# Performance work log

Hardware: AMD Instinct MI355X
Metric: run time of the kernel (lower is better)

The kernel has to match this reference:

```python
import jax, jax.numpy as jnp
import numpy as np

EMBED = 1024
HEADS = 16
HEAD_DIM = EMBED // HEADS
HIDDEN = int(EMBED * 4.0)
EPS = 1e-6


def setup_inputs() -> dict:
    key = jax.random.key(0)
    ks = jax.random.split(key, 8)
    s = lambda fan_in: 1.0 / np.sqrt(fan_in)
    x = jax.random.normal(ks[0], (2, 2048, EMBED), dtype=jnp.float32)
    return {
        "x": x,
        "ln1_g": jnp.ones((EMBED,), jnp.float32),
        "ln1_b": jnp.zeros((EMBED,), jnp.float32),
        "w_qkv": jax.random.normal(ks[1], (EMBED, 3 * EMBED), jnp.float32) * s(EMBED),
        "b_qkv": jnp.zeros((3 * EMBED,), jnp.float32),
        "w_proj": jax.random.normal(ks[2], (EMBED, EMBED), jnp.float32) * s(EMBED),
        "b_proj": jnp.zeros((EMBED,), jnp.float32),
        "ln2_g": jnp.ones((EMBED,), jnp.float32),
        "ln2_b": jnp.zeros((EMBED,), jnp.float32),
        "w_fc1": jax.random.normal(ks[3], (EMBED, HIDDEN), jnp.float32) * s(EMBED),
        "b_fc1": jnp.zeros((HIDDEN,), jnp.float32),
        "w_fc2": jax.random.normal(ks[4], (HIDDEN, EMBED), jnp.float32) * s(HIDDEN),
        "b_fc2": jnp.zeros((EMBED,), jnp.float32),
    }


def _layernorm(x, g, b):
    mu = jnp.mean(x, axis=-1, keepdims=True)
    var = jnp.mean(jnp.square(x - mu), axis=-1, keepdims=True)
    return (x - mu) * jax.lax.rsqrt(var + EPS) * g + b


def _attention(x, w_qkv, b_qkv, w_proj, b_proj):
    B, N, C = x.shape
    qkv = x @ w_qkv + b_qkv                      # [B,N,3C]
    qkv = qkv.reshape(B, N, 3, HEADS, HEAD_DIM)
    q, k, v = (qkv[:, :, 0], qkv[:, :, 1], qkv[:, :, 2])  # [B,N,H,Dh]
    scale = HEAD_DIM ** -0.5
    attn = jnp.einsum('bnhd,bmhd->bhnm', q, k) * scale     # [B,H,N,N]
    attn = jax.nn.softmax(attn, axis=-1)
    out = jnp.einsum('bhnm,bmhd->bnhd', attn, v).reshape(B, N, C)
    return out @ w_proj + b_proj


def reference(x, ln1_g, ln1_b, w_qkv, b_qkv, w_proj, b_proj,
              ln2_g, ln2_b, w_fc1, b_fc1, w_fc2, b_fc2):
    x = x + _attention(_layernorm(x, ln1_g, ln1_b), w_qkv, b_qkv, w_proj, b_proj)
    h = _layernorm(x, ln2_g, ln2_b)
    h = jax.nn.gelu(h @ w_fc1 + b_fc1, approximate=False)
    x = x + (h @ w_fc2 + b_fc2)
    return x
```

## Files before the change

### kernel.cpp

```cpp
#include <hip/hip_runtime.h>
#include <hip/hip_bf16.h>
#include <math.h>

typedef __bf16 bf16x8 __attribute__((ext_vector_type(8)));
typedef __bf16 bf16x4 __attribute__((ext_vector_type(4)));
typedef unsigned short u16x8 __attribute__((ext_vector_type(8)));
typedef float f32x4 __attribute__((ext_vector_type(4)));

#define EP_QKV 0
#define EP_GELU 1
#define EP_RES 2

static __device__ __forceinline__ unsigned short f2bf(float x) {
  unsigned int u = __float_as_uint(x);
  unsigned int r = (u + 0x7fffu + ((u >> 16) & 1u)) >> 16;
  return (unsigned short)r;
}

static __device__ __forceinline__ unsigned int pkbf(float lo, float hi) {
  return __builtin_amdgcn_perm(__float_as_uint(hi), __float_as_uint(lo), 0x07060302);
}

static __device__ __forceinline__ void async16(const void* g, void* l) {
  __builtin_amdgcn_global_load_lds((__attribute__((address_space(1))) void*)g,
                                   (__attribute__((address_space(3))) void*)l, 16, 0, 0);
}

__global__ __launch_bounds__(256) void wt_transpose(const float* __restrict__ in,
                                                    unsigned short* __restrict__ out,
                                                    int K, int N) {
  __shared__ float tile[32][33];
  const int n0 = blockIdx.x * 32;
  const int k0 = blockIdx.y * 32;
  const int tx = threadIdx.x;
  const int ty = threadIdx.y;
  #pragma unroll
  for (int i = ty; i < 32; i += 8)
    tile[i][tx] = in[(size_t)(k0 + i) * N + n0 + tx];
  __syncthreads();
  #pragma unroll
  for (int i = ty; i < 32; i += 8)
    out[(size_t)(n0 + i) * K + k0 + tx] = f2bf(tile[tx][i]);
}

__global__ __launch_bounds__(256) void ln_kernel(const float* __restrict__ x,
                                                 const float* __restrict__ g,
                                                 const float* __restrict__ b,
                                                 unsigned short* __restrict__ outp) {
  const int row = blockIdx.x;
  const int tid = threadIdx.x;
  const int wave = tid >> 6, lane = tid & 63;
  const float4 v = ((const float4*)(x + (size_t)row * 1024))[tid];
  float s = v.x + v.y + v.z + v.w;
  #pragma unroll
  for (int i = 1; i < 64; i <<= 1) s += __shfl_xor(s, i);
  __shared__ float red[4];
  if (lane == 0) red[wave] = s;
  __syncthreads();
  const float mean = (red[0] + red[1] + red[2] + red[3]) * (1.f / 1024.f);
  const float dx = v.x - mean, dy = v.y - mean, dz = v.z - mean, dw = v.w - mean;
  float ss = dx * dx + dy * dy + dz * dz + dw * dw;
  #pragma unroll
  for (int i = 1; i < 64; i <<= 1) ss += __shfl_xor(ss, i);
  __syncthreads();
  if (lane == 0) red[wave] = ss;
  __syncthreads();
  const float var = (red[0] + red[1] + red[2] + red[3]) * (1.f / 1024.f);
  const float inv = rsqrtf(var + 1e-6f);
  const float4 gv = ((const float4*)g)[tid];
  const float4 bv = ((const float4*)b)[tid];
  ushort4 o;
  o.x = f2bf(dx * inv * gv.x + bv.x);
  o.y = f2bf(dy * inv * gv.y + bv.y);
  o.z = f2bf(dz * inv * gv.z + bv.z);
  o.w = f2bf(dw * inv * gv.w + bv.w);
  ((ushort4*)(outp + (size_t)row * 1024))[tid] = o;
}

template <int TN, int BK>
__global__ __launch_bounds__(256) void gemm_kernel(
    const unsigned short* __restrict__ A,
    const unsigned short* __restrict__ BT,
    const float* __restrict__ bias,
    int M, int N, int K, int mode,
    void* __restrict__ outp, const float* __restrict__ res) {
  constexpr int AM = (TN == 128) ? 4 : 2;
  constexpr int ACH = BK / 16;
  constexpr int BCH = TN * BK / 2048;
  constexpr int CPR = BK / 8;
  constexpr int ABYTES = 256 * BK;
  constexpr int BBYTES = TN * BK * 2;
  __shared__ __align__(16) char smem[2 * (ABYTES + BBYTES)];

  const int tid = threadIdx.x;
  const int wave = tid >> 6, lane = tid & 63;
  const int quad = lane >> 4, l16 = lane & 15;
  const int wm = (TN == 128) ? (wave >> 1) : wave;
  const int wn = (TN == 128) ? (wave & 1) : 0;

  const int nbm = M >> 7, nbn = N / TN;
  const int lin = blockIdx.y * gridDim.x + blockIdx.x;
  const int g = lin & 7, idx = lin >> 3;
  const int gm = nbm >> 2, gn = nbn >> 1;
  const int bm = (g & 3) * gm + (idx % gm);
  const int bn = (g >> 2) * gn + (idx / gm);
  const int row_m = bm * 128, row_n = bn * TN;

  int ar[ACH], ac[ACH];
  #pragma unroll
  for (int i = 0; i < ACH; ++i) {
    const int c = wave * (64 * ACH) + i * 64 + lane;
    ar[i] = c / CPR;
    ac[i] = ((c % CPR) ^ (ar[i] & (CPR - 1))) * 8;
  }
  int br[BCH], bc[BCH];
  #pragma unroll
  for (int i = 0; i < BCH; ++i) {
    const int c = wave * (64 * BCH) + i * 64 + lane;
    br[i] = c / CPR;
    bc[i] = ((c % CPR) ^ (br[i] & (CPR - 1))) * 8;
  }

  const unsigned short* Ag = A + (size_t)row_m * K;
  const unsigned short* Bg = BT + (size_t)row_n * K;

  const f32x4 z = {0.f, 0.f, 0.f, 0.f};
  f32x4 acc[AM][4];
  #pragma unroll
  for (int i = 0; i < AM; ++i)
    #pragma unroll
    for (int j = 0; j < 4; ++j) acc[i][j] = z;

  auto issue = [&](int kt, int b) {
    unsigned short* As = (unsigned short*)(smem + b * ABYTES);
    unsigned short* Bs = (unsigned short*)(smem + 2 * ABYTES + b * BBYTES);
    #pragma unroll
    for (int i = 0; i < ACH; ++i)
      async16(Ag + (size_t)ar[i] * K + kt + ac[i], As + wave * (ACH * 512) + i * 512);
    #pragma unroll
    for (int i = 0; i < BCH; ++i)
      async16(Bg + (size_t)br[i] * K + kt + bc[i], Bs + wave * (BCH * 512) + i * 512);
  };

  issue(0, 0);
  for (int kt = 0; kt < K; kt += BK) {
    const int b = (kt / BK) & 1;
    __syncthreads();
    if (kt + BK < K) issue(kt + BK, b ^ 1);
    const unsigned short* As = (const unsigned short*)(smem + b * ABYTES);
    const unsigned short* Bs = (const unsigned short*)(smem + 2 * ABYTES + b * BBYTES);
    #pragma unroll
    for (int h = 0; h < BK / 32; ++h) {
      bf16x8 af[AM], bfv[4];
      #pragma unroll
      for (int t = 0; t < AM; ++t) {
        const int row = wm * (AM * 16) + t * 16 + l16;
        const int ch = (h * 4 + quad) ^ (row & (CPR - 1));
        af[t] = *(const bf16x8*)(As + row * BK + ch * 8);
      }
      #pragma unroll
      for (int t = 0; t < 4; ++t) {
        const int row = wn * 64 + t * 16 + l16;
        const int ch = (h * 4 + quad) ^ (row & (CPR - 1));
        bfv[t] = *(const bf16x8*)(Bs + row * BK + ch * 8);
      }
      #pragma unroll
      for (int tm = 0; tm < AM; ++tm)
        #pragma unroll
        for (int tn = 0; tn < 4; ++tn)
          acc[tm][tn] = __builtin_amdgcn_mfma_f32_16x16x32_bf16(af[tm], bfv[tn], acc[tm][tn], 0, 0, 0);
    }
  }

  #pragma unroll
  for (int tn = 0; tn < 4; ++tn) {
    const int col = row_n + wn * 64 + tn * 16 + l16;
    const float bv = bias[col];
    #pragma unroll
    for (int tm = 0; tm < AM; ++tm) {
      const int rbase = row_m + wm * (AM * 16) + tm * 16 + quad * 4;
      float v[4];
      #pragma unroll
      for (int r = 0; r < 4; ++r) v[r] = acc[tm][tn][r] + bv;
      if (mode == EP_QKV) {
        unsigned short* outw = (unsigned short*)outp;
        const int which = col >> 10;
        const int h = (col >> 6) & 15, d = col & 63;
        const int bb = rbase >> 11, n = rbase & 2047;
        const size_t bh = (size_t)(bb * 16 + h);
        if (which == 0) {
          #pragma unroll
          for (int r = 0; r < 4; ++r)
            outw[(bh * 2048 + n + r) * 64 + d] = f2bf(v[r] * 0.18033688011112043f);
        } else if (which == 1) {
          #pragma unroll
          for (int r = 0; r < 4; ++r)
            outw[4194304ull + (bh * 2048 + n + r) * 64 + d] = f2bf(v[r]);
        } else {
          uint2 o;
          o.x = pkbf(v[0], v[1]);
          o.y = pkbf(v[2], v[3]);
          *(uint2*)(outw + 8388608ull + (bh * 64 + d) * 2048 + n) = o;
        }
      } else if (mode == EP_GELU) {
        #pragma unroll
        for (int r = 0; r < 4; ++r) {
          const float u = v[r];
          const float c = 1.5957691216f * fmaf(0.044715f * u * u, u, u);
          const float e = __expf(c);
          const float gl = u - __fdividef(u, e + 1.0f);
          ((unsigned short*)outp)[(size_t)(rbase + r) * N + col] = f2bf(gl);
        }
      } else {
        #pragma unroll
        for (int r = 0; r < 4; ++r)
          ((float*)outp)[(size_t)(rbase + r) * N + col] =
              res[(size_t)(rbase + r) * N + col] + v[r];
      }
    }
  }
}

__global__ __launch_bounds__(256) void attn_kernel(
    const unsigned short* __restrict__ Q,
    const unsigned short* __restrict__ Kb,
    const unsigned short* __restrict__ VT,
    unsigned short* __restrict__ outp) {
  __shared__ __align__(16) char smem[73728];
  unsigned short* Qs = (unsigned short*)smem;
  unsigned short* Ks = (unsigned short*)(smem + 8192);
  unsigned short* Vs = (unsigned short*)(smem + 40960);

  const int tid = threadIdx.x;
  const int wave = tid >> 6, lane = tid & 63;
  const int quad = lane >> 4, l16 = lane & 15;

  const int lin = blockIdx.y * gridDim.x + blockIdx.x;
  const int g = lin & 7, idx = lin >> 3;
  const int bhi = g * 4 + (idx >> 5);
  const int q0 = (idx & 31) * 64;

  const unsigned short* Qg = Q + ((size_t)bhi * 2048 + q0) * 64;
  const unsigned short* Kg = Kb + (size_t)bhi * 2048 * 64;
  const unsigned short* Vg = VT + (size_t)bhi * 64 * 2048;

  {
    const int c0 = wave * 128 + lane;
    const int r0 = c0 >> 3, k0 = ((c0 & 7) ^ (r0 & 7)) * 8;
    const int c1 = c0 + 64;
    const int r1 = c1 >> 3, k1 = ((c1 & 7) ^ (r1 & 7)) * 8;
    async16(Qg + r0 * 64 + k0, Qs + wave * 1024);
    async16(Qg + r1 * 64 + k1, Qs + wave * 1024 + 512);
  }

  const unsigned short* kp[4];
  const unsigned short* vp[4];
  #pragma unroll
  for (int i = 0; i < 4; ++i) {
    const int c = wave * 256 + i * 64 + lane;
    const int krr = c >> 3, kcc = ((c & 7) ^ (krr & 7)) * 8;
    const int vrr = c >> 4, vcc = ((c & 15) ^ (vrr & 15)) * 8;
    kp[i] = Kg + (size_t)krr * 64 + kcc;
    vp[i] = Vg + (size_t)vrr * 2048 + vcc;
  }

  auto issueKV = [&](int b) {
    unsigned short* Kd = Ks + b * 8192;
    unsigned short* Vd = Vs + b * 8192;
    #pragma unroll
    for (int i = 0; i < 4; ++i) async16(kp[i], Kd + wave * 2048 + i * 512);
    #pragma unroll
    for (int i = 0; i < 4; ++i) async16(vp[i], Vd + wave * 2048 + i * 512);
    #pragma unroll
    for (int i = 0; i < 4; ++i) { kp[i] += 8192; vp[i] += 128; }
  };

  issueKV(0);
  __syncthreads();

  bf16x8 qb[4][2];
  #pragma unroll
  for (int nt = 0; nt < 4; ++nt)
    #pragma unroll
    for (int h = 0; h < 2; ++h) {
      const int row = nt * 16 + l16;
      const int ch = (h * 4 + quad) ^ (row & 7);
      qb[nt][h] = *(const bf16x8*)(Qs + row * 64 + ch * 8);
    }

  const f32x4 z = {0.f, 0.f, 0.f, 0.f};
  f32x4 acc[4][4];
  #pragma unroll
  for (int i = 0; i < 4; ++i)
    #pragma unroll
    for (int j = 0; j < 4; ++j) acc[i][j] = z;
  float lsum[4] = {0.f, 0.f, 0.f, 0.f};

  const int rowA = wave * 16 + l16;
  const int rowB = 64 + rowA;
  const int swk = l16 & 7;
  const float C2 = 23.083120654223414f;

  auto compute = [&](int b) {
    const unsigned short* Ksb = Ks + b * 8192;
    const unsigned short* Vsb = Vs + b * 8192;
    f32x4 sA[4], sB[4];
    #pragma unroll
    for (int nt = 0; nt < 4; ++nt) { sA[nt] = z; sB[nt] = z; }
    #pragma unroll
    for (int h = 0; h < 2; ++h) {
      const int ch = (h * 4 + quad) ^ swk;
      bf16x8 kfA = *(const bf16x8*)(Ksb + rowA * 64 + ch * 8);
      bf16x8 kfB = *(const bf16x8*)(Ksb + rowB * 64 + ch * 8);
      #pragma unroll
      for (int nt = 0; nt < 4; ++nt) {
        sA[nt] = __builtin_amdgcn_mfma_f32_16x16x32_bf16(kfA, qb[nt][h], sA[nt], 0, 0, 0);
        sB[nt] = __builtin_amdgcn_mfma_f32_16x16x32_bf16(kfB, qb[nt][h], sB[nt], 0, 0, 0);
      }
    }
    bf16x8 pb[4];
    #pragma unroll
    for (int nt = 0; nt < 4; ++nt) {
      union { unsigned int d[4]; bf16x8 b; } cv;
      float pa[4], pv[4];
      float ls = 0.f;
      #pragma unroll
      for (int r = 0; r < 4; ++r) {
        pa[r] = __builtin_amdgcn_exp2f(sA[nt][r] - C2);
        pv[r] = __builtin_amdgcn_exp2f(sB[nt][r] - C2);
        ls += pa[r] + pv[r];
      }
      cv.d[0] = pkbf(pa[0], pa[1]);
      cv.d[1] = pkbf(pa[2], pa[3]);
      cv.d[2] = pkbf(pv[0], pv[1]);
      cv.d[3] = pkbf(pv[2], pv[3]);
      lsum[nt] += ls;
      pb[nt] = cv.b;
    }
    #pragma unroll
    for (int mt = 0; mt < 4; ++mt) {
      const int d = mt * 16 + l16;
      const int cA = (wave * 2 + (quad >> 1)) ^ (d & 15);
      const int cB = (8 + wave * 2 + (quad >> 1)) ^ (d & 15);
      const int sub = (quad & 1) * 4;
      bf16x4 vA = *(const bf16x4*)(Vsb + d * 128 + cA * 8 + sub);
      bf16x4 vB = *(const bf16x4*)(Vsb + d * 128 + cB * 8 + sub);
      bf16x8 vf = __builtin_shufflevector(vA, vB, 0, 1, 2, 3, 4, 5, 6, 7);
      #pragma unroll
      for (int nt = 0; nt < 4; ++nt)
        acc[mt][nt] = __builtin_amdgcn_mfma_f32_16x16x32_bf16(vf, pb[nt], acc[mt][nt], 0, 0, 0);
    }
  };

  issueKV(1);
  compute(0);
  for (int t = 1; t < 16; ++t) {
    const int b = t & 1;
    __syncthreads();
    if (t + 1 < 16) issueKV(b ^ 1);
    compute(b);
  }
  __syncthreads();

  float* sc = (float*)smem;
  float* lred = (float*)(smem + 32768);
  #pragma unroll
  for (int nt = 0; nt < 4; ++nt) {
    float ls = lsum[nt];
    ls += __shfl_xor(ls, 16);
    ls += __shfl_xor(ls, 32);
    if (quad == 0) lred[wave * 64 + nt * 16 + l16] = ls;
  }
  if (wave >= 2) {
    float* dst = sc + (wave - 2) * 4096;
    #pragma unroll
    for (int mt = 0; mt < 4; ++mt)
      #pragma unroll
      for (int nt = 0; nt < 4; ++nt)
        *(f32x4*)(dst + (mt * 4 + nt) * 256 + lane * 4) = acc[mt][nt];
  }
  __syncthreads();
  if (wave < 2) {
    const float* src = sc + wave * 4096;
    #pragma unroll
    for (int mt = 0; mt < 4; ++mt)
      #pragma unroll
      for (int nt = 0; nt < 4; ++nt)
        acc[mt][nt] += *(const f32x4*)(src + (mt * 4 + nt) * 256 + lane * 4);
  }
  if (wave == 1) {
    float* dst = sc + 4096;
    #pragma unroll
    for (int mt = 0; mt < 4; ++mt)
      #pragma unroll
      for (int nt = 0; nt < 4; ++nt)
        *(f32x4*)(dst + (mt * 4 + nt) * 256 + lane * 4) = acc[mt][nt];
  }
  __syncthreads();
  if (wave == 0) {
    const float* src = sc + 4096;
    float linv[4];
    #pragma unroll
    for (int nt = 0; nt < 4; ++nt) {
      const int qi = nt * 16 + l16;
      const float l = lred[qi] + lred[64 + qi] + lred[128 + qi] + lred[192 + qi];
      linv[nt] = 1.0f / l;
    }
    const int b = bhi >> 4, h = bhi & 15;
    #pragma unroll
    for (int mt = 0; mt < 4; ++mt)
      #pragma unroll
      for (int nt = 0; nt < 4; ++nt) {
        f32x4 o = acc[mt][nt] + *(const f32x4*)(src + (mt * 4 + nt) * 256 + lane * 4);
        uint2 ov;
        ov.x = pkbf(o[0] * linv[nt], o[1] * linv[nt]);
        ov.y = pkbf(o[2] * linv[nt], o[3] * linv[nt]);
        *(uint2*)(outp + ((size_t)(b * 2048 + q0 + nt * 16 + l16)) * 1024 +
                  h * 64 + mt * 16 + quad * 4) = ov;
      }
  }
}

extern "C" void kernel_launch(void* const* d_in, const int* in_sizes, int n_in,
                              void* d_out, int out_size, void* d_ws, size_t ws_size,
                              hipStream_t stream) {
  (void)in_sizes; (void)n_in; (void)out_size; (void)ws_size;
  const float* x      = (const float*)d_in[0];
  const float* ln1_g  = (const float*)d_in[1];
  const float* ln1_b  = (const float*)d_in[2];
  const float* w_qkv  = (const float*)d_in[3];
  const float* b_qkv  = (const float*)d_in[4];
  const float* w_proj = (const float*)d_in[5];
  const float* b_proj = (const float*)d_in[6];
  const float* ln2_g  = (const float*)d_in[7];
  const float* ln2_b  = (const float*)d_in[8];
  const float* w_fc1  = (const float*)d_in[9];
  const float* b_fc1  = (const float*)d_in[10];
  const float* w_fc2  = (const float*)d_in[11];
  const float* b_fc2  = (const float*)d_in[12];

  char* ws = (char*)d_ws;
  unsigned short* wqkvT  = (unsigned short*)(ws + 0);
  unsigned short* wprojT = (unsigned short*)(ws + 6291456);
  unsigned short* wfc1T  = (unsigned short*)(ws + 8388608);
  unsigned short* wfc2T  = (unsigned short*)(ws + 16777216);
  unsigned short* lnb    = (unsigned short*)(ws + 25165824);
  unsigned short* qkvb   = (unsigned short*)(ws + 33554432);
  unsigned short* attnb  = (unsigned short*)(ws + 58720256);
  float*          x2     = (float*)(ws + 67108864);
  unsigned short* hbuf   = qkvb;

  dim3 tb(32, 8);
  wt_transpose<<<dim3(96, 32), tb, 0, stream>>>(w_qkv, wqkvT, 1024, 3072);
  wt_transpose<<<dim3(32, 32), tb, 0, stream>>>(w_proj, wprojT, 1024, 1024);
  wt_transpose<<<dim3(128, 32), tb, 0, stream>>>(w_fc1, wfc1T, 1024, 4096);
  wt_transpose<<<dim3(32, 128), tb, 0, stream>>>(w_fc2, wfc2T, 4096, 1024);

  ln_kernel<<<4096, 256, 0, stream>>>(x, ln1_g, ln1_b, lnb);

  gemm_kernel<128, 64><<<dim3(24, 32), 256, 0, stream>>>(lnb, wqkvT, b_qkv, 4096, 3072, 1024,
                                                         EP_QKV, (void*)qkvb, nullptr);

  attn_kernel<<<dim3(32, 32), 256, 0, stream>>>(qkvb, qkvb + 4194304, qkvb + 8388608, attnb);

  gemm_kernel<64, 64><<<dim3(16, 32), 256, 0, stream>>>(attnb, wprojT, b_proj, 4096, 1024, 1024,
                                                        EP_RES, (void*)x2, x);

  ln_kernel<<<4096, 256, 0, stream>>>(x2, ln2_g, ln2_b, lnb);

  gemm_kernel<128, 64><<<dim3(32, 32), 256, 0, stream>>>(lnb, wfc1T, b_fc1, 4096, 4096, 1024,
                                                         EP_GELU, (void*)hbuf, nullptr);

  gemm_kernel<64, 64><<<dim3(16, 32), 256, 0, stream>>>(hbuf, wfc2T, b_fc2, 4096, 1024, 4096,
                                                        EP_RES, d_out, x2);
}
```

Before: 334.7 us.

## Single-buffer V and load Q from global to fit three attention blocks per CU

The attention kernel shrinks its shared memory from 72KB to 48KB so three blocks can be resident per CU. It drops the Q staging buffer and loads Q fragments straight from global memory, keeps K double-buffered and makes V single-buffered. Each iteration now issues V and the next K, computes QK/softmax, then uses an explicit waitcnt plus barrier before the PV step. The cost is an extra barrier per tile, V load latency that is less hidden, and a final K prefetch that reads one tile past the current head.

Result: no change. 338.3 us (+1.1%).

```diff
diff --git a/kernel.cpp b/kernel.cpp
--- a/kernel.cpp
+++ b/kernel.cpp
@@ -221,15 +221,14 @@
   }
 }
 
-__global__ __launch_bounds__(256) void attn_kernel(
+__global__ __launch_bounds__(256, 3) void attn_kernel(
     const unsigned short* __restrict__ Q,
     const unsigned short* __restrict__ Kb,
     const unsigned short* __restrict__ VT,
     unsigned short* __restrict__ outp) {
-  __shared__ __align__(16) char smem[73728];
-  unsigned short* Qs = (unsigned short*)smem;
-  unsigned short* Ks = (unsigned short*)(smem + 8192);
-  unsigned short* Vs = (unsigned short*)(smem + 40960);
+  __shared__ __align__(16) char smem[49152];
+  unsigned short* Ks = (unsigned short*)smem;
+  unsigned short* Vs = (unsigned short*)(smem + 32768);
 
   const int tid = threadIdx.x;
   const int wave = tid >> 6, lane = tid & 63;
@@ -243,15 +242,6 @@
   const unsigned short* Qg = Q + ((size_t)bhi * 2048 + q0) * 64;
   const unsigned short* Kg = Kb + (size_t)bhi * 2048 * 64;
   const unsigned short* Vg = VT + (size_t)bhi * 64 * 2048;
-
-  {
-    const int c0 = wave * 128 + lane;
-    const int r0 = c0 >> 3, k0 = ((c0 & 7) ^ (r0 & 7)) * 8;
-    const int c1 = c0 + 64;
-    const int r1 = c1 >> 3, k1 = ((c1 & 7) ^ (r1 & 7)) * 8;
-    async16(Qg + r0 * 64 + k0, Qs + wave * 1024);
-    async16(Qg + r1 * 64 + k1, Qs + wave * 1024 + 512);
-  }
 
   const unsigned short* kp[4];
   const unsigned short* vp[4];
@@ -264,29 +254,28 @@
     vp[i] = Vg + (size_t)vrr * 2048 + vcc;
   }
 
-  auto issueKV = [&](int b) {
+  auto issueK = [&](int b) {
     unsigned short* Kd = Ks + b * 8192;
-    unsigned short* Vd = Vs + b * 8192;
     #pragma unroll
     for (int i = 0; i < 4; ++i) async16(kp[i], Kd + wave * 2048 + i * 512);
     #pragma unroll
-    for (int i = 0; i < 4; ++i) async16(vp[i], Vd + wave * 2048 + i * 512);
-    #pragma unroll
-    for (int i = 0; i < 4; ++i) { kp[i] += 8192; vp[i] += 128; }
+    for (int i = 0; i < 4; ++i) kp[i] += 8192;
   };
-
-  issueKV(0);
-  __syncthreads();
+  auto issueV = [&]() {
+    #pragma unroll
+    for (int i = 0; i < 4; ++i) async16(vp[i], Vs + wave * 2048 + i * 512);
+    #pragma unroll
+    for (int i = 0; i < 4; ++i) vp[i] += 128;
+  };
+
+  issueK(0);
 
   bf16x8 qb[4][2];
   #pragma unroll
   for (int nt = 0; nt < 4; ++nt)
     #pragma unroll
-    for (int h = 0; h < 2; ++h) {
-      const int row = nt * 16 + l16;
-      const int ch = (h * 4 + quad) ^ (row & 7);
-      qb[nt][h] = *(const bf16x8*)(Qs + row * 64 + ch * 8);
-    }
+    for (int h = 0; h < 2; ++h)
+      qb[nt][h] = *(const bf16x8*)(Qg + (nt * 16 + l16) * 64 + (h * 4 + quad) * 8);
 
   const f32x4 z = {0.f, 0.f, 0.f, 0.f};
   f32x4 acc[4][4];
@@ -301,9 +290,9 @@
   const int swk = l16 & 7;
   const float C2 = 23.083120654223414f;
 
-  auto compute = [&](int b) {
+  bf16x8 pb[4];
+  auto computeQK = [&](int b) {
     const unsigned short* Ksb = Ks + b * 8192;
-    const unsigned short* Vsb = Vs + b * 8192;
     f32x4 sA[4], sB[4];
     #pragma unroll
     for (int nt = 0; nt < 4; ++nt) { sA[nt] = z; sB[nt] = z; }
@@ -318,7 +307,6 @@
         sB[nt] = __builtin_amdgcn_mfma_f32_16x16x32_bf16(kfB, qb[nt][h], sB[nt], 0, 0, 0);
       }
     }
-    bf16x8 pb[4];
     #pragma unroll
     for (int nt = 0; nt < 4; ++nt) {
       union { unsigned int d[4]; bf16x8 b; } cv;
@@ -337,14 +325,17 @@
       lsum[nt] += ls;
       pb[nt] = cv.b;
     }
+  };
+
+  auto computePV = [&]() {
     #pragma unroll
     for (int mt = 0; mt < 4; ++mt) {
       const int d = mt * 16 + l16;
       const int cA = (wave * 2 + (quad >> 1)) ^ (d & 15);
       const int cB = (8 + wave * 2 + (quad >> 1)) ^ (d & 15);
       const int sub = (quad & 1) * 4;
-      bf16x4 vA = *(const bf16x4*)(Vsb + d * 128 + cA * 8 + sub);
-      bf16x4 vB = *(const bf16x4*)(Vsb + d * 128 + cB * 8 + sub);
+      bf16x4 vA = *(const bf16x4*)(Vs + d * 128 + cA * 8 + sub);
+      bf16x4 vB = *(const bf16x4*)(Vs + d * 128 + cB * 8 + sub);
       bf16x8 vf = __builtin_shufflevector(vA, vB, 0, 1, 2, 3, 4, 5, 6, 7);
       #pragma unroll
       for (int nt = 0; nt < 4; ++nt)
@@ -352,13 +343,13 @@
     }
   };
 
-  issueKV(1);
-  compute(0);
-  for (int t = 1; t < 16; ++t) {
-    const int b = t & 1;
+  for (int t = 0; t < 16; ++t) {
     __syncthreads();
-    if (t + 1 < 16) issueKV(b ^ 1);
-    compute(b);
+    issueV();
+    issueK((t + 1) & 1);
+    computeQK(t & 1);
+    asm volatile("s_waitcnt vmcnt(4) lgkmcnt(0)\n\ts_barrier" ::: "memory");
+    computePV();
   }
   __syncthreads();
 
```
